# Kernel optimization log

Measured on AMD Instinct MI355X. Metric: run time of the kernel, lower is better.

## Reference

```python
import jax, jax.numpy as jnp
import numpy as np

D = 20            # doc / proto-action feature dim (hard-coded via .view(slate_size, 20))
SLATE = 5
K = 100           # neighbors per slate element
N_DOCS = 1_000_000
HID = 256
SLOPE = 0.01      # F.leaky_relu default negative slope


def setup_inputs() -> dict:
    key = jax.random.key(0)
    ks = jax.random.split(key, 6)
    def lin_w(k, out_d, in_d):
        # kaiming-ish scale, matches torch Linear init magnitude roughly
        return jax.random.uniform(k, (out_d, in_d), jnp.float32, -1.0, 1.0) / np.sqrt(in_d)
    return {
        "input_state": jax.random.normal(ks[0], (D,), jnp.float32),
        "candidate_docs": jax.random.normal(ks[1], (N_DOCS, D), jnp.float32),
        "W1": lin_w(ks[2], HID, D),
        "b1": jnp.zeros((HID,), jnp.float32),
        "W2": lin_w(ks[3], HID, HID),
        "b2": jnp.zeros((HID,), jnp.float32),
        "W3": lin_w(ks[4], SLATE * D, HID),
        "b3": jnp.zeros((SLATE * D,), jnp.float32),
    }


def reference(input_state, candidate_docs, W1, b1, W2, b2, W3, b3):
    # --- actor policy net: Linear -> leaky_relu, x3 (leaky_relu also on output, as in source) ---
    x = input_state
    for W, b in ((W1, b1), (W2, b2), (W3, b3)):
        x = jax.nn.leaky_relu(x @ W.T + b, negative_slope=SLOPE)
    proto_slate = x.reshape(SLATE, D)                       # [slate, 20]

    # --- per-slate-element L2 distance to every candidate doc, vectorized ---
    # dists[s, n] = ||candidate_docs[n] - proto_slate[s]||_2
    diff = candidate_docs[None, :, :] - proto_slate[:, None, :]   # [slate, N, 20]
    dists = jnp.sqrt(jnp.sum(diff * diff, axis=-1))               # [slate, N]

    # top-k smallest distances (replaces full argsort + slice in the source)
    _, idx = jax.lax.top_k(-dists, K)                             # [slate, K]
    indices_tensor = idx.reshape(-1)                              # [slate*K], concat order as in source
    candidates_tensor = candidate_docs[indices_tensor]            # [slate*K, 20]
    return candidates_tensor, indices_tensor
```

## Files before the change

kernel.cpp:

```cpp
#include <hip/hip_runtime.h>
#include <stdint.h>
#include <math.h>

#define DDIM    20
#define SLATE   5
#define KSEL    100
#define HID     256
#define SAMPN   16384
#define NSH     8
#define SHCAP   1024
#define RCAP    8192
#define STP     128
#define OUT_IDX_OFF (SLATE * KSEL * DDIM)

#define WS_PROTO   0
#define WS_PROTOF  1024
#define WS_TP2     1536
#define WS_TM2     1556
#define WS_THI     1576
#define WS_SHCNT   1600
#define WS_STRICT  4160
#define WS_CNT2    6720
#define WS_ZEND    7040
#define WS_SKEYS   8192
#define WS_CAND    172032
#define WS_CAND2   335872
#define WS_STD2    499712
#define WS_STIX    540672
#define WS_STLEN   561152

__device__ __forceinline__ double dleaky(double x) { return x >= 0.0 ? x : 0.01 * x; }

__device__ __forceinline__ double calc_d2(const float* doc, const double* p) {
    double acc = 0.0;
#pragma unroll
    for (int i = 0; i < DDIM; ++i) {
        double d = (double)doc[i] - p[i];
        acc = fma(d, d, acc);
    }
    return acc;
}

__device__ __forceinline__ void load_doc(const float* __restrict__ docs,
                                         size_t n, float* doc) {
    const float4* dp = (const float4*)(docs + n * DDIM);
    float4 v0 = dp[0], v1 = dp[1], v2 = dp[2], v3 = dp[3], v4 = dp[4];
    doc[0] = v0.x; doc[1] = v0.y; doc[2] = v0.z; doc[3] = v0.w;
    doc[4] = v1.x; doc[5] = v1.y; doc[6] = v1.z; doc[7] = v1.w;
    doc[8] = v2.x; doc[9] = v2.y; doc[10] = v2.z; doc[11] = v2.w;
    doc[12] = v3.x; doc[13] = v3.y; doc[14] = v3.z; doc[15] = v3.w;
    doc[16] = v4.x; doc[17] = v4.y; doc[18] = v4.z; doc[19] = v4.w;
}

__device__ __forceinline__ int slate_use_primary(
    const unsigned* __restrict__ shardCnt, const unsigned* __restrict__ strictSh,
    int s) {
    unsigned strictTot = 0; bool ovf = false;
    for (int sh = 0; sh < NSH; ++sh) {
        if (shardCnt[(sh * SLATE + s) * 16] > SHCAP) ovf = true;
        strictTot += strictSh[(sh * SLATE + s) * 16];
    }
    return (strictTot >= KSEL) && !ovf;
}

__global__ __launch_bounds__(256) void mlp_sample_kernel(
    const float* __restrict__ x0, const float* __restrict__ docs,
    const float* __restrict__ W1, const float* __restrict__ b1,
    const float* __restrict__ W2, const float* __restrict__ b2,
    const float* __restrict__ W3, const float* __restrict__ b3,
    double* __restrict__ proto, float* __restrict__ protof,
    unsigned short* __restrict__ skeys, unsigned* __restrict__ zeroBase, int N) {
    const int bid = blockIdx.x, t = threadIdx.x;
    if (bid == SAMPN / 256) {
        for (int i = t; i < 1360; i += 256) zeroBase[i] = 0u;
        return;
    }
    __shared__ double xs[DDIM];
    __shared__ double h1[HID];
    __shared__ double h2[HID];
    __shared__ double ps[SLATE * DDIM];
    if (t < DDIM) xs[t] = (double)x0[t];
    __syncthreads();
    {
        double acc = 0.0;
#pragma unroll
        for (int i = 0; i < DDIM; ++i) acc = fma(xs[i], (double)W1[t * DDIM + i], acc);
        acc += (double)b1[t];
        h1[t] = dleaky(acc);
    }
    __syncthreads();
    {
        double acc = 0.0;
        for (int i = 0; i < HID; ++i) acc = fma(h1[i], (double)W2[t * HID + i], acc);
        acc += (double)b2[t];
        h2[t] = dleaky(acc);
    }
    __syncthreads();
    if (t < SLATE * DDIM) {
        double acc = 0.0;
        for (int i = 0; i < HID; ++i) acc = fma(h2[i], (double)W3[t * HID + i], acc);
        acc += (double)b3[t];
        double v = dleaky(acc);
        ps[t] = v;
        if (bid == 0) { proto[t] = v; protof[t] = (float)v; }
    }
    __syncthreads();
    int i = bid * 256 + t;
    if (i < SAMPN && i < N) {
        float doc[DDIM];
        load_doc(docs, (size_t)i, doc);
#pragma unroll
        for (int s = 0; s < SLATE; ++s) {
            double d2 = calc_d2(doc, ps + s * DDIM);
            skeys[s * SAMPN + i] = (unsigned short)(__float_as_uint((float)d2) >> 16);
        }
    }
}

__global__ __launch_bounds__(1024) void select_kernel(
    const unsigned short* __restrict__ skeys,
    unsigned short* __restrict__ Tp2, unsigned short* __restrict__ Tm2,
    unsigned short* __restrict__ Thi) {
    int s = blockIdx.x, t = threadIdx.x;
    int lane = t & 63, w = t >> 6;
    __shared__ unsigned wsum[2][16];
    const unsigned* kp = (const unsigned*)(skeys + (size_t)s * SAMPN);
    unsigned kw[8];
#pragma unroll
    for (int j = 0; j < 8; ++j) kw[j] = kp[j * 1024 + t];

    unsigned X10 = 0, X100 = 0;
    int buf = 0;
    for (int b = 15; b >= 0; --b) {
        unsigned p10 = X10 | (1u << b), p100 = X100 | (1u << b);
        int c10 = 0, c100 = 0;
#pragma unroll
        for (int j = 0; j < 8; ++j) {
            unsigned lo = kw[j] & 0xffffu, hi = kw[j] >> 16;
            c10  += (lo < p10)  + (hi < p10);
            c100 += (lo < p100) + (hi < p100);
        }
#pragma unroll
        for (int off = 32; off; off >>= 1) {
            c10  += __shfl_down(c10, off);
            c100 += __shfl_down(c100, off);
        }
        if (lane == 0) wsum[buf][w] = (unsigned)c10 | ((unsigned)c100 << 16);
        __syncthreads();
        unsigned t10 = 0, t100 = 0;
        for (int i = 0; i < 16; ++i) {
            unsigned v = wsum[buf][i];
            t10 += v & 0xffffu; t100 += v >> 16;
        }
        if ((int)t10 < 10)   X10 = p10;
        if ((int)t100 < 100) X100 = p100;
        buf ^= 1;
    }
    if (t == 0) {
        unsigned tp = X10 + 2u; if (tp > 65535u) tp = 65535u;
        Tp2[s] = (unsigned short)tp;
        Tm2[s] = (unsigned short)(X10 >= 2u ? X10 - 2u : 0u);
        Thi[s] = (unsigned short)X100;
    }
}

__global__ __launch_bounds__(256) void compact1_kernel(
    const float* __restrict__ docs, const float* __restrict__ protof,
    const unsigned short* __restrict__ Tp2, const unsigned short* __restrict__ Tm2,
    unsigned* __restrict__ shardCnt, unsigned* __restrict__ strictSh,
    unsigned* __restrict__ candIdx, int N) {
    __shared__ float psf[SLATE * DDIM];
    __shared__ unsigned short ktp[SLATE], ktm[SLATE];
    int t = threadIdx.x;
    if (t < SLATE * DDIM) psf[t] = protof[t];
    if (t < SLATE) { ktp[t] = Tp2[t]; ktm[t] = Tm2[t]; }
    __syncthreads();

    int n = blockIdx.x * 256 + t;
    bool dv = n < N;
    int lane = t & 63;
    int sh = blockIdx.x & (NSH - 1);

    float doc[DDIM];
    if (dv) load_doc(docs, (size_t)n, doc);
    else {
#pragma unroll
        for (int i = 0; i < DDIM; ++i) doc[i] = 0.f;
    }
    float acc[SLATE] = {0.f, 0.f, 0.f, 0.f, 0.f};
#pragma unroll
    for (int i = 0; i < DDIM; ++i) {
        float dvi = doc[i];
#pragma unroll
        for (int s = 0; s < SLATE; ++s) {
            float d = dvi - psf[s * DDIM + i];
            acc[s] = fmaf(d, d, acc[s]);
        }
    }
#pragma unroll
    for (int s = 0; s < SLATE; ++s) {
        unsigned k32 = __float_as_uint(acc[s]) >> 16;
        bool hit = dv && k32 <= (unsigned)ktp[s];
        unsigned long long ms = __ballot(dv && k32 <= (unsigned)ktm[s]);
        if (ms) {
            int ldr = __ffsll(ms) - 1;
            if (lane == ldr)
                atomicAdd(&strictSh[(sh * SLATE + s) * 16], (unsigned)__popcll(ms));
        }
        unsigned long long mh = __ballot(hit);
        if (mh) {
            int ldr = __ffsll(mh) - 1;
            unsigned base = 0;
            if (lane == ldr)
                base = atomicAdd(&shardCnt[(sh * SLATE + s) * 16], (unsigned)__popcll(mh));
            base = __shfl(base, ldr);
            if (hit) {
                unsigned pos = base + (unsigned)__popcll(mh & ((1ull << lane) - 1ull));
                if (pos < SHCAP)
                    candIdx[((size_t)(s * NSH + sh)) * SHCAP + pos] = (unsigned)n;
            }
        }
    }
}

__global__ __launch_bounds__(256) void rank_fused_kernel(
    const float* __restrict__ docs, const double* __restrict__ proto,
    const unsigned short* __restrict__ Thi,
    const unsigned* __restrict__ shardCnt, const unsigned* __restrict__ strictSh,
    const unsigned* __restrict__ candIdx, unsigned* __restrict__ rscratch,
    double* __restrict__ stD2, unsigned* __restrict__ stIx,
    unsigned* __restrict__ stLen, unsigned* __restrict__ doneCnt,
    float* __restrict__ out, int N) {
    const int sh = blockIdx.x, s = blockIdx.y, t = threadIdx.x;
    __shared__ double   ld[SHCAP];
    __shared__ unsigned li[SHCAP];
    __shared__ double   ps[DDIM];
    __shared__ double   outD2[KSEL];
    __shared__ unsigned outIx[KSEL];
    __shared__ unsigned Ls[NSH], offs[NSH + 1];
    __shared__ unsigned c_s, rcnt;
    __shared__ int      prim_s, last_s;

    if (t < DDIM) ps[t] = proto[s * DDIM + t];
    if (t == 0) { prim_s = slate_use_primary(shardCnt, strictSh, s); rcnt = 0u; }
    __syncthreads();

    unsigned c;
    if (prim_s) {
        if (t == 0) {
            unsigned cc = shardCnt[(sh * SLATE + s) * 16];
            c_s = cc > SHCAP ? SHCAP : cc;
        }
        __syncthreads();
        c = c_s;
        const unsigned* src = candIdx + ((size_t)(s * NSH + sh)) * SHCAP;
        for (unsigned i = t; i < c; i += 256) {
            unsigned idx = src[i];
            li[i] = idx;
            float doc[DDIM];
            load_doc(docs, (size_t)idx, doc);
            ld[i] = calc_d2(doc, ps);
        }
    } else {
        unsigned kt = Thi[s];
        unsigned* lst = rscratch + (size_t)s * RCAP + (size_t)sh * SHCAP;
        int lo = (int)((long long)N * sh / NSH);
        int hi = (int)((long long)N * (sh + 1) / NSH);
        for (int n = lo + t; n < hi; n += 256) {
            float doc[DDIM];
            load_doc(docs, (size_t)n, doc);
            double d2 = calc_d2(doc, ps);
            unsigned key = __float_as_uint((float)d2) >> 16;
            if (key <= kt) {
                unsigned pos = atomicAdd(&rcnt, 1u);
                if (pos < SHCAP) lst[pos] = (unsigned)n;
            }
        }
        __syncthreads();
        c = rcnt < SHCAP ? rcnt : SHCAP;
        for (unsigned i = t; i < c; i += 256) {
            unsigned idx = lst[i];
            li[i] = idx;
            float doc[DDIM];
            load_doc(docs, (size_t)idx, doc);
            ld[i] = calc_d2(doc, ps);
        }
    }
    __syncthreads();

    for (unsigned e = t; e < c; e += 256) {
        double de = ld[e]; unsigned ie = li[e];
        unsigned rank = 0;
        for (unsigned j = 0; j < c; ++j) {
            double dj = ld[j]; unsigned ij = li[j];
            rank += (dj < de) || (dj == de && ij < ie);
        }
        if (rank < KSEL) { outD2[rank] = de; outIx[rank] = ie; }
    }
    __syncthreads();

    unsigned L = c < KSEL ? c : KSEL;
    size_t base = (size_t)(s * NSH + sh) * STP;
    for (unsigned r = t; r < L; r += 256) {
        stD2[base + r] = outD2[r];
        stIx[base + r] = outIx[r];
    }
    if (t == 0) stLen[s * NSH + sh] = L;

    __threadfence();
    __syncthreads();
    if (t == 0) {
        unsigned old = atomicAdd(&doneCnt[s * 16], 1u);
        last_s = (old == NSH - 1);
    }
    __syncthreads();
    if (!last_s) return;
    __threadfence();

    if (t < NSH) Ls[t] = stLen[s * NSH + t];
    __syncthreads();
    if (t == 0) {
        unsigned o = 0;
        for (int so = 0; so < NSH; ++so) { offs[so] = o; o += Ls[so]; }
        offs[NSH] = o;
    }
    __syncthreads();
    for (int so = 0; so < NSH; ++so) {
        unsigned Lx = Ls[so];
        for (unsigned i = t; i < Lx; i += 256) {
            ld[so * KSEL + i] = stD2[(size_t)(s * NSH + so) * STP + i];
            li[so * KSEL + i] = stIx[(size_t)(s * NSH + so) * STP + i];
        }
    }
    __syncthreads();

    unsigned S = offs[NSH];
    for (unsigned e = t; e < S; e += 256) {
        int so = 0;
        while (e >= offs[so + 1]) ++so;
        unsigned i = e - offs[so];
        double xd = ld[so * KSEL + i];
        unsigned xi = li[so * KSEL + i];
        unsigned rank = i;
        for (int so2 = 0; so2 < NSH; ++so2) {
            if (so2 == so) continue;
            unsigned lo = 0, hi = Ls[so2];
            while (lo < hi) {
                unsigned mid = (lo + hi) >> 1;
                double dj = ld[so2 * KSEL + mid];
                unsigned ij = li[so2 * KSEL + mid];
                bool less = (dj < xd) || (dj == xd && ij < xi);
                if (less) lo = mid + 1; else hi = mid;
            }
            rank += lo;
        }
        if (rank < KSEL) outIx[rank] = xi;
    }
    __syncthreads();

    if (t < KSEL) out[(size_t)OUT_IDX_OFF + s * KSEL + t] = (float)outIx[t];
    for (int pos = t; pos < KSEL * DDIM; pos += 256) {
        int r = pos / DDIM, cc = pos % DDIM;
        out[((size_t)s * KSEL + r) * DDIM + cc] = docs[(size_t)outIx[r] * DDIM + cc];
    }
}

extern "C" void kernel_launch(void* const* d_in, const int* in_sizes, int n_in,
                              void* d_out, int out_size, void* d_ws, size_t ws_size,
                              hipStream_t stream) {
    const float* x0   = (const float*)d_in[0];
    const float* docs = (const float*)d_in[1];
    const float* W1   = (const float*)d_in[2];
    const float* b1   = (const float*)d_in[3];
    const float* W2   = (const float*)d_in[4];
    const float* b2   = (const float*)d_in[5];
    const float* W3   = (const float*)d_in[6];
    const float* b3   = (const float*)d_in[7];
    int N = in_sizes[1] / DDIM;

    char* ws = (char*)d_ws;
    double*         proto    = (double*)(ws + WS_PROTO);
    float*          protof   = (float*)(ws + WS_PROTOF);
    unsigned short* Tp2      = (unsigned short*)(ws + WS_TP2);
    unsigned short* Tm2      = (unsigned short*)(ws + WS_TM2);
    unsigned short* Thi      = (unsigned short*)(ws + WS_THI);
    unsigned*       shardCnt = (unsigned*)(ws + WS_SHCNT);
    unsigned*       strictSh = (unsigned*)(ws + WS_STRICT);
    unsigned*       doneCnt  = (unsigned*)(ws + WS_CNT2);
    unsigned short* skeys    = (unsigned short*)(ws + WS_SKEYS);
    unsigned*       candIdx  = (unsigned*)(ws + WS_CAND);
    unsigned*       rscratch = (unsigned*)(ws + WS_CAND2);
    double*         stD2     = (double*)(ws + WS_STD2);
    unsigned*       stIx     = (unsigned*)(ws + WS_STIX);
    unsigned*       stLen    = (unsigned*)(ws + WS_STLEN);
    float*          outp     = (float*)d_out;

    mlp_sample_kernel<<<SAMPN / 256 + 1, 256, 0, stream>>>(
        x0, docs, W1, b1, W2, b2, W3, b3, proto, protof, skeys, shardCnt, N);
    select_kernel<<<SLATE, 1024, 0, stream>>>(skeys, Tp2, Tm2, Thi);
    int nb = (N + 255) / 256;
    compact1_kernel<<<nb, 256, 0, stream>>>(docs, protof, Tp2, Tm2,
                                            shardCnt, strictSh, candIdx, N);
    rank_fused_kernel<<<dim3(NSH, SLATE), 256, 0, stream>>>(
        docs, proto, Thi, shardCnt, strictSh, candIdx, rscratch,
        stD2, stIx, stLen, doneCnt, outp, N);
}
```

Measured before the change: 106.9 us.

## Split fused rank into rank and merge kernels; unroll rank and interleave binary searches

Replaces the last-block-done atomic merge inside the rank kernel with a separate 1024-thread merge kernel launched per slate. The O(c^2) rank loop is unrolled by 8, and the merge runs the eight per-shard binary searches in lockstep to expose instruction-level parallelism. This drops the threadfence/atomic handshake and gives the merge more threads, at the cost of one extra kernel launch.

```diff
diff --git a/kernel.cpp b/kernel.cpp
--- a/kernel.cpp
+++ b/kernel.cpp
@@ -223,23 +223,21 @@
     }
 }
 
-__global__ __launch_bounds__(256) void rank_fused_kernel(
+__global__ __launch_bounds__(256) void rank_kernel(
     const float* __restrict__ docs, const double* __restrict__ proto,
     const unsigned short* __restrict__ Thi,
     const unsigned* __restrict__ shardCnt, const unsigned* __restrict__ strictSh,
     const unsigned* __restrict__ candIdx, unsigned* __restrict__ rscratch,
     double* __restrict__ stD2, unsigned* __restrict__ stIx,
-    unsigned* __restrict__ stLen, unsigned* __restrict__ doneCnt,
-    float* __restrict__ out, int N) {
+    unsigned* __restrict__ stLen, int N) {
     const int sh = blockIdx.x, s = blockIdx.y, t = threadIdx.x;
     __shared__ double   ld[SHCAP];
     __shared__ unsigned li[SHCAP];
     __shared__ double   ps[DDIM];
     __shared__ double   outD2[KSEL];
     __shared__ unsigned outIx[KSEL];
-    __shared__ unsigned Ls[NSH], offs[NSH + 1];
     __shared__ unsigned c_s, rcnt;
-    __shared__ int      prim_s, last_s;
+    __shared__ int      prim_s;
 
     if (t < DDIM) ps[t] = proto[s * DDIM + t];
     if (t == 0) { prim_s = slate_use_primary(shardCnt, strictSh, s); rcnt = 0u; }
@@ -291,7 +289,22 @@
     for (unsigned e = t; e < c; e += 256) {
         double de = ld[e]; unsigned ie = li[e];
         unsigned rank = 0;
-        for (unsigned j = 0; j < c; ++j) {
+        unsigned j = 0;
+        for (; j + 8 <= c; j += 8) {
+            double d0 = ld[j+0], d1 = ld[j+1], d2 = ld[j+2], d3 = ld[j+3];
+            double d4 = ld[j+4], d5 = ld[j+5], d6 = ld[j+6], d7 = ld[j+7];
+            unsigned i0 = li[j+0], i1 = li[j+1], i2 = li[j+2], i3 = li[j+3];
+            unsigned i4 = li[j+4], i5 = li[j+5], i6 = li[j+6], i7 = li[j+7];
+            rank += ((d0 < de) || (d0 == de && i0 < ie))
+                  + ((d1 < de) || (d1 == de && i1 < ie))
+                  + ((d2 < de) || (d2 == de && i2 < ie))
+                  + ((d3 < de) || (d3 == de && i3 < ie))
+                  + ((d4 < de) || (d4 == de && i4 < ie))
+                  + ((d5 < de) || (d5 == de && i5 < ie))
+                  + ((d6 < de) || (d6 == de && i6 < ie))
+                  + ((d7 < de) || (d7 == de && i7 < ie));
+        }
+        for (; j < c; ++j) {
             double dj = ld[j]; unsigned ij = li[j];
             rank += (dj < de) || (dj == de && ij < ie);
         }
@@ -306,62 +319,78 @@
         stIx[base + r] = outIx[r];
     }
     if (t == 0) stLen[s * NSH + sh] = L;
-
-    __threadfence();
-    __syncthreads();
-    if (t == 0) {
-        unsigned old = atomicAdd(&doneCnt[s * 16], 1u);
-        last_s = (old == NSH - 1);
-    }
-    __syncthreads();
-    if (!last_s) return;
-    __threadfence();
-
+}
+
+__global__ __launch_bounds__(1024) void merge_kernel(
+    const float* __restrict__ docs,
+    const double* __restrict__ stD2, const unsigned* __restrict__ stIx,
+    const unsigned* __restrict__ stLen, float* __restrict__ out) {
+    int s = blockIdx.x, t = threadIdx.x;
+    __shared__ double md[NSH * KSEL];
+    __shared__ unsigned mi[NSH * KSEL];
+    __shared__ unsigned Ls[NSH], offs[NSH + 1];
+    __shared__ unsigned sel[KSEL];
     if (t < NSH) Ls[t] = stLen[s * NSH + t];
     __syncthreads();
     if (t == 0) {
         unsigned o = 0;
-        for (int so = 0; so < NSH; ++so) { offs[so] = o; o += Ls[so]; }
+        for (int sh = 0; sh < NSH; ++sh) { offs[sh] = o; o += Ls[sh]; }
         offs[NSH] = o;
     }
     __syncthreads();
-    for (int so = 0; so < NSH; ++so) {
-        unsigned Lx = Ls[so];
-        for (unsigned i = t; i < Lx; i += 256) {
-            ld[so * KSEL + i] = stD2[(size_t)(s * NSH + so) * STP + i];
-            li[so * KSEL + i] = stIx[(size_t)(s * NSH + so) * STP + i];
+    for (int sh = 0; sh < NSH; ++sh) {
+        unsigned L = Ls[sh];
+        for (unsigned i = t; i < L; i += 1024) {
+            md[sh * KSEL + i] = stD2[(size_t)(s * NSH + sh) * STP + i];
+            mi[sh * KSEL + i] = stIx[(size_t)(s * NSH + sh) * STP + i];
         }
     }
     __syncthreads();
 
     unsigned S = offs[NSH];
-    for (unsigned e = t; e < S; e += 256) {
-        int so = 0;
-        while (e >= offs[so + 1]) ++so;
-        unsigned i = e - offs[so];
-        double xd = ld[so * KSEL + i];
-        unsigned xi = li[so * KSEL + i];
+    for (unsigned e = t; e < S; e += 1024) {
+        int sh = 0;
+        while (e >= offs[sh + 1]) ++sh;
+        unsigned i = e - offs[sh];
+        double xd = md[sh * KSEL + i];
+        unsigned xi = mi[sh * KSEL + i];
+        unsigned lo[NSH], hi[NSH];
+#pragma unroll
+        for (int so = 0; so < NSH; ++so) { lo[so] = 0; hi[so] = (so == sh) ? 0u : Ls[so]; }
+        bool active = true;
+        while (active) {
+            active = false;
+            double   dj[NSH];
+            unsigned ij[NSH], mid[NSH];
+#pragma unroll
+            for (int so = 0; so < NSH; ++so) {
+                if (lo[so] < hi[so]) {
+                    unsigned m = (lo[so] + hi[so]) >> 1;
+                    mid[so] = m;
+                    dj[so] = md[so * KSEL + m];
+                    ij[so] = mi[so * KSEL + m];
+                }
+            }
+#pragma unroll
+            for (int so = 0; so < NSH; ++so) {
+                if (lo[so] < hi[so]) {
+                    bool less = (dj[so] < xd) || (dj[so] == xd && ij[so] < xi);
+                    if (less) lo[so] = mid[so] + 1; else hi[so] = mid[so];
+                    if (lo[so] < hi[so]) active = true;
+                }
+            }
+        }
         unsigned rank = i;
-        for (int so2 = 0; so2 < NSH; ++so2) {
-            if (so2 == so) continue;
-            unsigned lo = 0, hi = Ls[so2];
-            while (lo < hi) {
-                unsigned mid = (lo + hi) >> 1;
-                double dj = ld[so2 * KSEL + mid];
-                unsigned ij = li[so2 * KSEL + mid];
-                bool less = (dj < xd) || (dj == xd && ij < xi);
-                if (less) lo = mid + 1; else hi = mid;
-            }
-            rank += lo;
-        }
-        if (rank < KSEL) outIx[rank] = xi;
-    }
-    __syncthreads();
-
-    if (t < KSEL) out[(size_t)OUT_IDX_OFF + s * KSEL + t] = (float)outIx[t];
-    for (int pos = t; pos < KSEL * DDIM; pos += 256) {
-        int r = pos / DDIM, cc = pos % DDIM;
-        out[((size_t)s * KSEL + r) * DDIM + cc] = docs[(size_t)outIx[r] * DDIM + cc];
+#pragma unroll
+        for (int so = 0; so < NSH; ++so) rank += lo[so];
+        if (rank < KSEL) sel[rank] = xi;
+    }
+    __syncthreads();
+
+    if (t < KSEL) out[(size_t)OUT_IDX_OFF + s * KSEL + t] = (float)sel[t];
+    for (int pos = t; pos < KSEL * DDIM; pos += 1024) {
+        int r = pos / DDIM, c = pos % DDIM;
+        out[((size_t)s * KSEL + r) * DDIM + c] = docs[(size_t)sel[r] * DDIM + c];
     }
 }
 
@@ -386,7 +415,6 @@
     unsigned short* Thi      = (unsigned short*)(ws + WS_THI);
     unsigned*       shardCnt = (unsigned*)(ws + WS_SHCNT);
     unsigned*       strictSh = (unsigned*)(ws + WS_STRICT);
-    unsigned*       doneCnt  = (unsigned*)(ws + WS_CNT2);
     unsigned short* skeys    = (unsigned short*)(ws + WS_SKEYS);
     unsigned*       candIdx  = (unsigned*)(ws + WS_CAND);
     unsigned*       rscratch = (unsigned*)(ws + WS_CAND2);
@@ -401,7 +429,8 @@
     int nb = (N + 255) / 256;
     compact1_kernel<<<nb, 256, 0, stream>>>(docs, protof, Tp2, Tm2,
                                             shardCnt, strictSh, candIdx, N);
-    rank_fused_kernel<<<dim3(NSH, SLATE), 256, 0, stream>>>(
+    rank_kernel<<<dim3(NSH, SLATE), 256, 0, stream>>>(
         docs, proto, Thi, shardCnt, strictSh, candIdx, rscratch,
-        stD2, stIx, stLen, doneCnt, outp, N);
-}
+        stD2, stIx, stLen, N);
+    merge_kernel<<<SLATE, 1024, 0, stream>>>(docs, stD2, stIx, stLen, outp);
+}
```

Result: faster. 92.38 us (-13.6%).
